# Kernel tuning notes

Hardware: AMD Instinct MI355X
Metric: run time of the kernel (lower is better)

The kernel has to match this reference:

```python
import jax, jax.numpy as jnp
import numpy as np

N, D_IN, WID, LAT, DPD, H, N_SEG = 131072, 128, 512, 512, 128, 8, 256


def cumulative_segment_mean(data, segment_ids):
    # prefix mean that resets at each new (sorted) segment id
    n = data.shape[0]
    idx = jnp.arange(n)
    seg_start = jnp.concatenate([jnp.ones((1,), bool), segment_ids[1:] != segment_ids[:-1]])
    # index of the first element of each token's segment
    start_idx = jax.lax.associative_scan(jnp.maximum, jnp.where(seg_start, idx, 0))
    cs = jnp.cumsum(data, axis=0)
    base = jnp.where((start_idx > 0)[:, None], cs[jnp.maximum(start_idx - 1, 0)], jnp.zeros((), data.dtype))
    count = (idx - start_idx + 1).astype(data.dtype)[:, None]
    return (cs - base) / count


def setup_inputs() -> dict:
    key = jax.random.key(0)
    ks = jax.random.split(key, 12)
    he = lambda k, sh: jax.random.normal(k, sh, jnp.float32) * np.sqrt(2.0 / sh[0]).astype(np.float32)
    inputs = jax.random.normal(ks[0], (N, D_IN), jnp.float32)
    segment_ids = jnp.sort(jax.random.randint(ks[1], (N,), 0, N_SEG, dtype=jnp.int64))
    return {
        "inputs": inputs,
        "segment_ids": segment_ids,
        "W1": he(ks[2], (D_IN, WID)), "b1": jnp.zeros((WID,), jnp.float32),
        "W2": he(ks[3], (WID, WID)), "b2": jnp.zeros((WID,), jnp.float32),
        "W3": he(ks[4], (WID, LAT)), "b3": jnp.zeros((LAT,), jnp.float32),
        "Wr": he(ks[5], (LAT, LAT)), "br": jnp.zeros((LAT,), jnp.float32),
        "W_k": he(ks[6], (LAT + D_IN, DPD * H)),
        "W_q": jax.random.normal(ks[7], (H, DPD), jnp.float32) * 0.05,
    }


def reference(inputs, segment_ids, W1, b1, W2, b2, W3, b3, Wr, br, W_k, W_q):
    relu = jax.nn.relu
    h = relu(inputs @ W1 + b1)          # psi layer 1
    h = relu(h @ W2 + b2)               # psi layer 2
    encoded = relu(h @ W3 + b3)         # psi latent projection
    agg = cumulative_segment_mean(encoded, segment_ids)
    agg = relu(agg @ Wr + br)           # rho
    combined = jnp.concatenate([inputs, agg], axis=-1)   # [N, D_IN+LAT]
    keys = (combined @ W_k).reshape(inputs.shape[0], H, DPD)  # split+stack heads
    preattn = jnp.einsum('nhd,hd->nh', keys, W_q) / jnp.sqrt(jnp.float32(DPD))
    return preattn
```

## Files before the change

kernel.cpp:

```cpp
#include <hip/hip_runtime.h>
#include <hip/hip_bf16.h>
#include <stdint.h>

typedef unsigned short ushortT;
typedef __bf16 bf16x8 __attribute__((ext_vector_type(8)));
typedef float f32x4 __attribute__((ext_vector_type(4)));
typedef unsigned short u16x8 __attribute__((ext_vector_type(8)));

#define N_TOK 131072
#define NSEG  256
#define RSPL  8

__device__ __forceinline__ uint32_t f2bf(float f) {
  union { float f; uint32_t u; } c; c.f = f;
  uint32_t u = c.u;
  u += 0x7fffu + ((u >> 16) & 1u);
  return u >> 16;
}
__device__ __forceinline__ float bf2f(uint32_t b) {
  union { uint32_t u; float f; } c; c.u = b << 16;
  return c.f;
}

__device__ __forceinline__ void gload_lds16(const void* g, void* l) {
  __builtin_amdgcn_global_load_lds(
      (const __attribute__((address_space(1))) void*)g,
      (__attribute__((address_space(3))) void*)l, 16, 0, 0);
}


__global__ void transpose_bf16_kernel(const float* __restrict__ W, ushortT* __restrict__ WT,
                                      int Kd, int Nd) {
  int i = blockIdx.x * 256 + threadIdx.x;
  if (i < Kd * Nd) {
    int n = i / Kd, k = i % Kd;
    WT[i] = (ushortT)f2bf(W[(size_t)k * Nd + n]);
  }
}

__global__ void weff_kernel(const float* __restrict__ Wk, const float* __restrict__ Wq,
                            float* __restrict__ weff) {
  const int c = blockIdx.x;
  const int lane = threadIdx.x;
  const float rs = 0.08838834764831845f;
#pragma unroll
  for (int h = 0; h < 8; ++h) {
    float acc = Wk[(size_t)c * 1024 + h * 128 + lane] * Wq[h * 128 + lane]
              + Wk[(size_t)c * 1024 + h * 128 + 64 + lane] * Wq[h * 128 + 64 + lane];
#pragma unroll
    for (int off = 32; off >= 1; off >>= 1) acc += __shfl_xor(acc, off, 64);
    if (lane == 0) weff[c * 8 + h] = acc * rs;
  }
}

__global__ void seg_bounds_kernel(const int* __restrict__ seg, int* __restrict__ gbnd) {
  const int s = (int)threadIdx.x + (int)blockIdx.x * 512;
  if (s > NSEG) return;
  int lo = 0, hi = N_TOK;
  while (lo < hi) { int m = (lo + hi) >> 1; if (seg[m] < s) lo = m + 1; else hi = m; }
  gbnd[s] = lo;
}


template <int K, bool RELU, bool BIAS, bool XF32>
__global__ __launch_bounds__(256, 2)
void gemm_m97_kernel(const void* __restrict__ Av, const ushortT* __restrict__ BT,
                     const float* __restrict__ bias, ushortT* __restrict__ C) {
  __shared__ ushortT lA[128 * 64];
  __shared__ ushortT lB[128 * 64];
  constexpr int NT = K / 64;

  const int nwg  = (int)gridDim.x;
  const int cpx  = nwg >> 3;
  const int flat = (int)blockIdx.x;
  const int swz  = (flat & 7) * cpx + (flat >> 3);
  const int bm   = swz >> 2;
  const int bn   = swz & 3;

  const int t = (int)threadIdx.x;
  const int w = t >> 6, lane = t & 63;
  const int wm = w >> 1, wn = w & 1;
  const int q = lane >> 4, lr = lane & 15;

  const int srow = t >> 3;
  const int slc  = (t & 7) ^ (srow & 7);

  const ushortT* Ab = nullptr;
  const float*   Xf = nullptr;
  if (XF32) Xf = (const float*)Av + (size_t)(bm * 128 + srow) * 128 + slc * 8;
  else      Ab = (const ushortT*)Av + (size_t)(bm * 128 + srow) * K + slc * 8;
  const ushortT* Bg = BT + (size_t)(bn * 128 + srow) * K + slc * 8;

  f32x4 acc[4][4];
#pragma unroll
  for (int i = 0; i < 4; ++i)
#pragma unroll
    for (int j = 0; j < 4; ++j) acc[i][j] = 0.f;

  const int cc0 = (q ^ (lr & 7)) << 4;
  const int cc1 = ((4 + q) ^ (lr & 7)) << 4;
  const char* lAc = (const char*)lA;
  const char* lBc = (const char*)lB;

#pragma unroll 1
  for (int kt = 0; kt < NT; ++kt) {
    if (XF32) {
      const float* src = Xf + kt * 64;
#pragma unroll
      for (int j = 0; j < 4; ++j) {
        const float4 v0 = *(const float4*)(src + (size_t)j * 32 * 128);
        const float4 v1 = *(const float4*)(src + (size_t)j * 32 * 128 + 4);
        uint4 pk;
        pk.x = f2bf(v0.x) | (f2bf(v0.y) << 16);
        pk.y = f2bf(v0.z) | (f2bf(v0.w) << 16);
        pk.z = f2bf(v1.x) | (f2bf(v1.y) << 16);
        pk.w = f2bf(v1.z) | (f2bf(v1.w) << 16);
        *(uint4*)((char*)lA + j * 4096 + t * 16) = pk;
      }
    } else {
      const ushortT* src = Ab + kt * 64;
#pragma unroll
      for (int j = 0; j < 4; ++j)
        gload_lds16(src + (size_t)j * 32 * K, (char*)lA + j * 4096 + t * 16);
    }
    {
      const ushortT* src = Bg + kt * 64;
#pragma unroll
      for (int j = 0; j < 4; ++j)
        gload_lds16(src + (size_t)j * 32 * K, (char*)lB + j * 4096 + t * 16);
    }
    __syncthreads();

    bf16x8 a0[4], a1[4], b0[4], b1[4];
#pragma unroll
    for (int m = 0; m < 4; ++m) {
      const int ro = (wm * 64 + m * 16 + lr) * 128;
      a0[m] = *(const bf16x8*)(lAc + ro + cc0);
      a1[m] = *(const bf16x8*)(lAc + ro + cc1);
    }
#pragma unroll
    for (int n = 0; n < 4; ++n) {
      const int ro = (wn * 64 + n * 16 + lr) * 128;
      b0[n] = *(const bf16x8*)(lBc + ro + cc0);
      b1[n] = *(const bf16x8*)(lBc + ro + cc1);
    }

    __builtin_amdgcn_s_setprio(1);
#pragma unroll
    for (int n = 0; n < 4; ++n)
#pragma unroll
      for (int m = 0; m < 4; ++m)
        acc[m][n] = __builtin_amdgcn_mfma_f32_16x16x32_bf16(a0[m], b0[n], acc[m][n], 0, 0, 0);
#pragma unroll
    for (int n = 0; n < 4; ++n)
#pragma unroll
      for (int m = 0; m < 4; ++m)
        acc[m][n] = __builtin_amdgcn_mfma_f32_16x16x32_bf16(a1[m], b1[n], acc[m][n], 0, 0, 0);
    __builtin_amdgcn_s_setprio(0);

    __syncthreads();
  }

  const int row0 = bm * 128 + wm * 64 + q * 4;
  const int col0 = bn * 128 + wn * 64 + lr;
#pragma unroll
  for (int n = 0; n < 4; ++n) {
    const int col = col0 + n * 16;
    const float bvv = BIAS ? bias[col] : 0.f;
#pragma unroll
    for (int m = 0; m < 4; ++m) {
#pragma unroll
      for (int r = 0; r < 4; ++r) {
        float v = acc[m][n][r] + bvv;
        if (RELU) v = fmaxf(v, 0.f);
        C[(size_t)(row0 + m * 16 + r) * 512 + col] = (ushortT)f2bf(v);
      }
    }
  }
}


__global__ __launch_bounds__(256)
void seg_sum_kernel(const ushortT* __restrict__ z, const int* __restrict__ gbnd,
                    float* __restrict__ part, int c0, int rows) {
  const int s  = (int)blockIdx.x >> 3;
  const int rg = (int)blockIdx.x & 7;
  const int t  = (int)threadIdx.x;

  const int gb0 = gbnd[s], gb1 = gbnd[s + 1];
  int beg = gb0 > c0 ? gb0 : c0;
  int end = gb1 < c0 + rows ? gb1 : c0 + rows;
  int len = end - beg; if (len < 0) len = 0;
  const int r0 = beg + ((len * rg) >> 3);
  const int r1 = beg + ((len * (rg + 1)) >> 3);

  float a0 = 0.f, a1 = 0.f;
  const uint32_t* __restrict__ zp = (const uint32_t*)z;
  int r = r0;
  for (; r + 8 <= r1; r += 8) {
    uint32_t v[8];
#pragma unroll
    for (int i = 0; i < 8; ++i) v[i] = zp[(size_t)(r + i - c0) * 256 + t];
#pragma unroll
    for (int i = 0; i < 8; ++i) { a0 += bf2f(v[i] & 0xffffu); a1 += bf2f(v[i] >> 16); }
  }
  for (; r < r1; ++r) {
    const uint32_t v = zp[(size_t)(r - c0) * 256 + t];
    a0 += bf2f(v & 0xffffu); a1 += bf2f(v >> 16);
  }
  float2 pv; pv.x = a0; pv.y = a1;
  ((float2*)part)[(s * 8 + rg) * 256 + t] = pv;
}

__global__ __launch_bounds__(256)
void seg_scan2_kernel(const ushortT* __restrict__ z, ushortT* __restrict__ gout,
                      const int* __restrict__ gbnd, const float* __restrict__ br,
                      const float* __restrict__ part,
                      const float* __restrict__ cin, float* __restrict__ cout,
                      int c0, int rows) {
  const int s  = (int)blockIdx.x >> 3;
  const int rg = (int)blockIdx.x & 7;
  const int t  = (int)threadIdx.x;

  const int gb0 = gbnd[s], gb1 = gbnd[s + 1];
  int beg = gb0 > c0 ? gb0 : c0;
  int end = gb1 < c0 + rows ? gb1 : c0 + rows;
  int len = end - beg; if (len < 0) len = 0;
  const int r0 = beg + ((len * rg) >> 3);
  const int r1 = beg + ((len * (rg + 1)) >> 3);

  const float2 cv = ((const float2*)cin)[s * 256 + t];
  float a0 = cv.x, a1 = cv.y;
  for (int q2 = 0; q2 < rg; ++q2) {
    const float2 pv = ((const float2*)part)[(s * 8 + q2) * 256 + t];
    a0 += pv.x; a1 += pv.y;
  }
  int cb = c0 - gb0; if (cb < 0) cb = 0;
  const int seglen = gb1 - gb0; if (cb > seglen) cb = seglen;
  const int cnt0 = cb + (r0 - beg);

  const float b0 = br[2 * t], b1v = br[2 * t + 1];
  const uint32_t* __restrict__ zp = (const uint32_t*)z;
  uint32_t* __restrict__ gp = (uint32_t*)gout;

  int r = r0;
  for (; r + 8 <= r1; r += 8) {
    uint32_t v[8];
#pragma unroll
    for (int i = 0; i < 8; ++i) v[i] = zp[(size_t)(r + i - c0) * 256 + t];
#pragma unroll
    for (int i = 0; i < 8; ++i) {
      a0 += bf2f(v[i] & 0xffffu);
      a1 += bf2f(v[i] >> 16);
      const float inv = 1.0f / (float)(cnt0 + (r + i) - r0 + 1);
      const float g0 = fmaxf(fmaf(a0, inv, b0), 0.f);
      const float g1 = fmaxf(fmaf(a1, inv, b1v), 0.f);
      gp[(size_t)(r + i - c0) * 256 + t] = f2bf(g0) | (f2bf(g1) << 16);
    }
  }
  for (; r < r1; ++r) {
    const uint32_t v = zp[(size_t)(r - c0) * 256 + t];
    a0 += bf2f(v & 0xffffu);
    a1 += bf2f(v >> 16);
    const float inv = 1.0f / (float)(cnt0 + r - r0 + 1);
    const float g0 = fmaxf(fmaf(a0, inv, b0), 0.f);
    const float g1 = fmaxf(fmaf(a1, inv, b1v), 0.f);
    gp[(size_t)(r - c0) * 256 + t] = f2bf(g0) | (f2bf(g1) << 16);
  }

  if (rg == 7) {
    float2 co; co.x = a0; co.y = a1;
    ((float2*)cout)[s * 256 + t] = co;
  }
}


__global__ __launch_bounds__(256)
void final_kernel(const float* __restrict__ X, const ushortT* __restrict__ g,
                  const float* __restrict__ weff, float* __restrict__ out, int rows) {
  const int t = (int)threadIdx.x;
  const int wv = t >> 6, lane = t & 63;

  float wx0[8], wx1[8], wg[8][8];
#pragma unroll
  for (int h = 0; h < 8; ++h) {
    wx0[h] = weff[(2 * lane) * 8 + h];
    wx1[h] = weff[(2 * lane + 1) * 8 + h];
  }
#pragma unroll
  for (int j = 0; j < 8; ++j)
#pragma unroll
    for (int h = 0; h < 8; ++h)
      wg[j][h] = weff[(128 + 8 * lane + j) * 8 + h];

  for (int row = (int)blockIdx.x * 4 + wv; row < rows; row += (int)gridDim.x * 4) {
    const float2 xv = *(const float2*)&X[(size_t)row * 128 + 2 * lane];
    const u16x8 gv = *(const u16x8*)&g[(size_t)row * 512 + 8 * lane];
    float pp[8];
#pragma unroll
    for (int h = 0; h < 8; ++h) pp[h] = xv.x * wx0[h] + xv.y * wx1[h];
#pragma unroll
    for (int j = 0; j < 8; ++j) {
      const float f = bf2f((uint32_t)gv[j]);
#pragma unroll
      for (int h = 0; h < 8; ++h) pp[h] = fmaf(f, wg[j][h], pp[h]);
    }
#pragma unroll
    for (int off = 32; off >= 1; off >>= 1) {
#pragma unroll
      for (int h = 0; h < 8; ++h) pp[h] += __shfl_xor(pp[h], off, 64);
    }
    if (lane == 0) {
#pragma unroll
      for (int h = 0; h < 8; ++h) out[(size_t)row * 8 + h] = pp[h];
    }
  }
}


extern "C" void kernel_launch(void* const* d_in, const int* in_sizes, int n_in,
                              void* d_out, int out_size, void* d_ws, size_t ws_size,
                              hipStream_t stream) {
  const float* X  = (const float*)d_in[0];
  const int*   sg = (const int*)d_in[1];
  const float* W1 = (const float*)d_in[2];
  const float* b1 = (const float*)d_in[3];
  const float* W2 = (const float*)d_in[4];
  const float* b2 = (const float*)d_in[5];
  const float* W3 = (const float*)d_in[6];
  const float* b3 = (const float*)d_in[7];
  const float* Wr = (const float*)d_in[8];
  const float* br = (const float*)d_in[9];
  const float* Wk = (const float*)d_in[10];
  const float* Wq = (const float*)d_in[11];
  float* out = (float*)d_out;

  const size_t szW1T  = 512 * 128 * 2;
  const size_t szWT   = 512 * 512 * 2;
  const size_t szWeff = 640 * 8 * 4;
  const size_t szPart = (size_t)NSEG * RSPL * 256 * 2 * 4;
  const size_t szCar  = (size_t)NSEG * 256 * 2 * 4;
  const size_t szBnd  = (NSEG + 1) * 4;
  const size_t fixed  = szW1T + 3 * szWT + szWeff + szPart + 2 * szCar + szBnd + 256;

  int CH = 0;
  const int cands[6] = {131072, 65536, 32768, 16384, 8192, 4096};
  for (int i = 0; i < 6; ++i) {
    const size_t need = fixed + 2 * (size_t)cands[i] * 512 * 2;
    if (need <= ws_size) { CH = cands[i]; break; }
  }
  if (CH == 0) CH = 4096;

  char* p = (char*)d_ws;
  ushortT* W1T  = (ushortT*)p; p += szW1T;
  ushortT* W2T  = (ushortT*)p; p += szWT;
  ushortT* W3T  = (ushortT*)p; p += szWT;
  ushortT* WrT  = (ushortT*)p; p += szWT;
  float*   weff = (float*)p;   p += szWeff;
  float*   part = (float*)p;   p += szPart;
  float*   carA = (float*)p;   p += szCar;
  float*   carB = (float*)p;   p += szCar;
  int*     gbnd = (int*)p;     p += (szBnd + 255) & ~255ull;
  ushortT* p1   = (ushortT*)p; p += (size_t)CH * 512 * 2;
  ushortT* p2   = (ushortT*)p;

  transpose_bf16_kernel<<<(512 * 128 + 255) / 256, 256, 0, stream>>>(W1, W1T, 128, 512);
  transpose_bf16_kernel<<<(512 * 512 + 255) / 256, 256, 0, stream>>>(W2, W2T, 512, 512);
  transpose_bf16_kernel<<<(512 * 512 + 255) / 256, 256, 0, stream>>>(W3, W3T, 512, 512);
  transpose_bf16_kernel<<<(512 * 512 + 255) / 256, 256, 0, stream>>>(Wr, WrT, 512, 512);
  weff_kernel<<<640, 64, 0, stream>>>(Wk, Wq, weff);
  seg_bounds_kernel<<<1, 512, 0, stream>>>(sg, gbnd);
  hipMemsetAsync(carA, 0, szCar, stream);

  int par = 0;
  for (int c0 = 0; c0 < N_TOK; c0 += CH) {
    const int gG = (CH / 128) * 4;
    const int gF = (CH / 4 < 4096) ? CH / 4 : 4096;
    float* cin  = par ? carB : carA;
    float* cout = par ? carA : carB;
    gemm_m97_kernel<128, true,  true,  true ><<<gG, 256, 0, stream>>>(X + (size_t)c0 * 128, W1T, b1, p1);
    gemm_m97_kernel<512, true,  true,  false><<<gG, 256, 0, stream>>>(p1, W2T, b2, p2);
    gemm_m97_kernel<512, true,  true,  false><<<gG, 256, 0, stream>>>(p2, W3T, b3, p1);
    gemm_m97_kernel<512, false, false, false><<<gG, 256, 0, stream>>>(p1, WrT, nullptr, p2);
    seg_sum_kernel <<<NSEG * RSPL, 256, 0, stream>>>(p2, gbnd, part, c0, CH);
    seg_scan2_kernel<<<NSEG * RSPL, 256, 0, stream>>>(p2, p1, gbnd, br, part,
                                                      cin, cout, c0, CH);
    final_kernel<<<gF, 256, 0, stream>>>(X + (size_t)c0 * 128, p1, weff,
                                         out + (size_t)c0 * 8, CH);
    par ^= 1;
  }
}
```

Measured before the change: 502.8 us.

## Compute final head projection with bf16 MFMA instead of scalar FMAs

Replaces the scalar-FMA final projection, which reduced across lanes with shuffles, with an MFMA 16x16x32 bf16 kernel. The effective weights are stored transposed in bf16, padded to 16 columns, and staged in LDS. Each wave computes 32 rows by loading X (converted to bf16) and the aggregated features directly as MFMA A operands. This removes the shuffle reduction and the heavy VALU work. In exchange, X and the weights are rounded to bf16, half the MFMA columns are wasted on padding, and the A-operand reads are strided per lane.

```diff
diff --git a/kernel.cpp b/kernel.cpp
--- a/kernel.cpp
+++ b/kernel.cpp
@@ -5,7 +5,6 @@
 typedef unsigned short ushortT;
 typedef __bf16 bf16x8 __attribute__((ext_vector_type(8)));
 typedef float f32x4 __attribute__((ext_vector_type(4)));
-typedef unsigned short u16x8 __attribute__((ext_vector_type(8)));
 
 #define N_TOK 131072
 #define NSEG  256
@@ -39,7 +38,7 @@
 }
 
 __global__ void weff_kernel(const float* __restrict__ Wk, const float* __restrict__ Wq,
-                            float* __restrict__ weff) {
+                            ushortT* __restrict__ weffT) {
   const int c = blockIdx.x;
   const int lane = threadIdx.x;
   const float rs = 0.08838834764831845f;
@@ -49,7 +48,10 @@
               + Wk[(size_t)c * 1024 + h * 128 + 64 + lane] * Wq[h * 128 + 64 + lane];
 #pragma unroll
     for (int off = 32; off >= 1; off >>= 1) acc += __shfl_xor(acc, off, 64);
-    if (lane == 0) weff[c * 8 + h] = acc * rs;
+    if (lane == 0) {
+      weffT[h * 640 + c]       = (ushortT)f2bf(acc * rs);
+      weffT[(h + 8) * 640 + c] = 0;
+    }
   }
 }
 
@@ -276,44 +278,55 @@
 
 
 __global__ __launch_bounds__(256)
-void final_kernel(const float* __restrict__ X, const ushortT* __restrict__ g,
-                  const float* __restrict__ weff, float* __restrict__ out, int rows) {
+void final_mfma_kernel(const float* __restrict__ X, const ushortT* __restrict__ g,
+                       const ushortT* __restrict__ weffT, float* __restrict__ out) {
+  __shared__ char lw[16 * 1296];
   const int t = (int)threadIdx.x;
+
+#pragma unroll
+  for (int i = 0; i < 5; ++i) {
+    const int idx = i * 256 + t;
+    const int row = idx / 80, c = idx % 80;
+    *(uint4*)(lw + row * 1296 + c * 16) =
+        *(const uint4*)((const char*)weffT + row * 1280 + c * 16);
+  }
+  __syncthreads();
+
   const int wv = t >> 6, lane = t & 63;
-
-  float wx0[8], wx1[8], wg[8][8];
-#pragma unroll
-  for (int h = 0; h < 8; ++h) {
-    wx0[h] = weff[(2 * lane) * 8 + h];
-    wx1[h] = weff[(2 * lane + 1) * 8 + h];
-  }
-#pragma unroll
-  for (int j = 0; j < 8; ++j)
-#pragma unroll
-    for (int h = 0; h < 8; ++h)
-      wg[j][h] = weff[(128 + 8 * lane + j) * 8 + h];
-
-  for (int row = (int)blockIdx.x * 4 + wv; row < rows; row += (int)gridDim.x * 4) {
-    const float2 xv = *(const float2*)&X[(size_t)row * 128 + 2 * lane];
-    const u16x8 gv = *(const u16x8*)&g[(size_t)row * 512 + 8 * lane];
-    float pp[8];
-#pragma unroll
-    for (int h = 0; h < 8; ++h) pp[h] = xv.x * wx0[h] + xv.y * wx1[h];
-#pragma unroll
-    for (int j = 0; j < 8; ++j) {
-      const float f = bf2f((uint32_t)gv[j]);
-#pragma unroll
-      for (int h = 0; h < 8; ++h) pp[h] = fmaf(f, wg[j][h], pp[h]);
-    }
-#pragma unroll
-    for (int off = 32; off >= 1; off >>= 1) {
-#pragma unroll
-      for (int h = 0; h < 8; ++h) pp[h] += __shfl_xor(pp[h], off, 64);
-    }
-    if (lane == 0) {
-#pragma unroll
-      for (int h = 0; h < 8; ++h) out[(size_t)row * 8 + h] = pp[h];
-    }
+  const int q = lane >> 4, lr = lane & 15;
+  const int rbase = (int)blockIdx.x * 128 + wv * 32;
+
+  f32x4 acc[2];
+  acc[0] = 0.f; acc[1] = 0.f;
+
+#pragma unroll
+  for (int kk = 0; kk < 20; ++kk) {
+    const bf16x8 b = *(const bf16x8*)(lw + lr * 1296 + kk * 64 + q * 16);
+#pragma unroll
+    for (int mt = 0; mt < 2; ++mt) {
+      const int row = rbase + mt * 16 + lr;
+      union { ushortT u[8]; bf16x8 v; } a;
+      if (kk < 4) {
+        const float* xr = X + (size_t)row * 128 + kk * 32 + q * 8;
+        const float4 v0 = *(const float4*)xr;
+        const float4 v1 = *(const float4*)(xr + 4);
+        a.u[0] = (ushortT)f2bf(v0.x); a.u[1] = (ushortT)f2bf(v0.y);
+        a.u[2] = (ushortT)f2bf(v0.z); a.u[3] = (ushortT)f2bf(v0.w);
+        a.u[4] = (ushortT)f2bf(v1.x); a.u[5] = (ushortT)f2bf(v1.y);
+        a.u[6] = (ushortT)f2bf(v1.z); a.u[7] = (ushortT)f2bf(v1.w);
+      } else {
+        a.v = *(const bf16x8*)(g + (size_t)row * 512 + (kk - 4) * 32 + q * 8);
+      }
+      acc[mt] = __builtin_amdgcn_mfma_f32_16x16x32_bf16(a.v, b, acc[mt], 0, 0, 0);
+    }
+  }
+
+  if (lr < 8) {
+#pragma unroll
+    for (int mt = 0; mt < 2; ++mt)
+#pragma unroll
+      for (int r = 0; r < 4; ++r)
+        out[(size_t)(rbase + mt * 16 + q * 4 + r) * 8 + lr] = acc[mt][r];
   }
 }
 
@@ -337,11 +350,11 @@
 
   const size_t szW1T  = 512 * 128 * 2;
   const size_t szWT   = 512 * 512 * 2;
-  const size_t szWeff = 640 * 8 * 4;
+  const size_t szWeff = 16 * 640 * 2;
   const size_t szPart = (size_t)NSEG * RSPL * 256 * 2 * 4;
   const size_t szCar  = (size_t)NSEG * 256 * 2 * 4;
   const size_t szBnd  = (NSEG + 1) * 4;
-  const size_t fixed  = szW1T + 3 * szWT + szWeff + szPart + 2 * szCar + szBnd + 256;
+  const size_t fixed  = szW1T + 3 * szWT + szWeff + szPart + 2 * szCar + szBnd + 512;
 
   int CH = 0;
   const int cands[6] = {131072, 65536, 32768, 16384, 8192, 4096};
@@ -352,30 +365,29 @@
   if (CH == 0) CH = 4096;
 
   char* p = (char*)d_ws;
-  ushortT* W1T  = (ushortT*)p; p += szW1T;
-  ushortT* W2T  = (ushortT*)p; p += szWT;
-  ushortT* W3T  = (ushortT*)p; p += szWT;
-  ushortT* WrT  = (ushortT*)p; p += szWT;
-  float*   weff = (float*)p;   p += szWeff;
-  float*   part = (float*)p;   p += szPart;
-  float*   carA = (float*)p;   p += szCar;
-  float*   carB = (float*)p;   p += szCar;
-  int*     gbnd = (int*)p;     p += (szBnd + 255) & ~255ull;
-  ushortT* p1   = (ushortT*)p; p += (size_t)CH * 512 * 2;
-  ushortT* p2   = (ushortT*)p;
+  ushortT* W1T   = (ushortT*)p; p += szW1T;
+  ushortT* W2T   = (ushortT*)p; p += szWT;
+  ushortT* W3T   = (ushortT*)p; p += szWT;
+  ushortT* WrT   = (ushortT*)p; p += szWT;
+  ushortT* weffT = (ushortT*)p; p += szWeff;
+  float*   part  = (float*)p;   p += szPart;
+  float*   carA  = (float*)p;   p += szCar;
+  float*   carB  = (float*)p;   p += szCar;
+  int*     gbnd  = (int*)p;     p += (szBnd + 255) & ~255ull;
+  ushortT* p1    = (ushortT*)p; p += (size_t)CH * 512 * 2;
+  ushortT* p2    = (ushortT*)p;
 
   transpose_bf16_kernel<<<(512 * 128 + 255) / 256, 256, 0, stream>>>(W1, W1T, 128, 512);
   transpose_bf16_kernel<<<(512 * 512 + 255) / 256, 256, 0, stream>>>(W2, W2T, 512, 512);
   transpose_bf16_kernel<<<(512 * 512 + 255) / 256, 256, 0, stream>>>(W3, W3T, 512, 512);
   transpose_bf16_kernel<<<(512 * 512 + 255) / 256, 256, 0, stream>>>(Wr, WrT, 512, 512);
-  weff_kernel<<<640, 64, 0, stream>>>(Wk, Wq, weff);
+  weff_kernel<<<640, 64, 0, stream>>>(Wk, Wq, weffT);
   seg_bounds_kernel<<<1, 512, 0, stream>>>(sg, gbnd);
   hipMemsetAsync(carA, 0, szCar, stream);
 
   int par = 0;
   for (int c0 = 0; c0 < N_TOK; c0 += CH) {
     const int gG = (CH / 128) * 4;
-    const int gF = (CH / 4 < 4096) ? CH / 4 : 4096;
     float* cin  = par ? carB : carA;
     float* cout = par ? carA : carB;
     gemm_m97_kernel<128, true,  true,  true ><<<gG, 256, 0, stream>>>(X + (size_t)c0 * 128, W1T, b1, p1);
@@ -385,8 +397,8 @@
     seg_sum_kernel <<<NSEG * RSPL, 256, 0, stream>>>(p2, gbnd, part, c0, CH);
     seg_scan2_kernel<<<NSEG * RSPL, 256, 0, stream>>>(p2, p1, gbnd, br, part,
                                                       cin, cout, c0, CH);
-    final_kernel<<<gF, 256, 0, stream>>>(X + (size_t)c0 * 128, p1, weff,
-                                         out + (size_t)c0 * 8, CH);
+    final_mfma_kernel<<<CH / 128, 256, 0, stream>>>(X + (size_t)c0 * 128, p1, weffT,
+                                                    out + (size_t)c0 * 8);
     par ^= 1;
   }
 }
```

Result: faster. 435.4 us (-13.4%).
